# Performance work log

Measured on AMD Instinct MI355X. Metric: run time of the kernel, lower is better.

Reference implementation:

```python
import jax, jax.numpy as jnp
import numpy as np

D, H, BS, K_TOP = 2560, 32, 32, 16
HD = D // H  # 80
B, S = 2, 1024
SCALE = HD ** -0.5


def setup_inputs() -> dict:
    key = jax.random.key(0)
    ks = jax.random.split(key, 10)
    sc = 0.02

    def lin(k, i, o):
        return (jax.random.normal(k, (i, o), jnp.float32) * sc,
                jnp.zeros((o,), jnp.float32))

    Wq, bq = lin(ks[0], D, D)
    Wk, bk = lin(ks[1], D, D)
    Wv, bv = lin(ks[2], D, D)
    Wo, bo = lin(ks[3], D, D)
    comp_W1, comp_b1 = lin(ks[4], BS * HD, 4 * HD)
    comp_W2, comp_b2 = lin(ks[5], 4 * HD, HD)
    comp_pos = jax.random.normal(ks[6], (BS, HD), jnp.float32) * sc
    gate_W1, gate_b1 = lin(ks[7], D, D // 2)
    gate_W2, gate_b2 = lin(ks[8], D // 2, 3)
    hidden_states = jax.random.normal(ks[9], (B, S, D), jnp.float32)
    return dict(hidden_states=hidden_states, Wq=Wq, bq=bq, Wk=Wk, bk=bk,
                Wv=Wv, bv=bv, Wo=Wo, bo=bo, comp_pos=comp_pos,
                comp_W1=comp_W1, comp_b1=comp_b1, comp_W2=comp_W2,
                comp_b2=comp_b2, gate_W1=gate_W1, gate_b1=gate_b1,
                gate_W2=gate_W2, gate_b2=gate_b2)


def reference(hidden_states, Wq, bq, Wk, bk, Wv, bv, Wo, bo, comp_pos,
              comp_W1, comp_b1, comp_W2, comp_b2, gate_W1, gate_b1,
              gate_W2, gate_b2):
    b, s, dm = hidden_states.shape
    blocks = s // BS

    def heads(y):  # [b,s,D] -> [b,H,s,hd]
        return y.reshape(b, s, H, HD).transpose(0, 2, 1, 3)

    q = heads(hidden_states @ Wq + bq)
    k = heads(hidden_states @ Wk + bk)
    v = heads(hidden_states @ Wv + bv)

    # --- compression branch: per-head block compression MLP (shared K/V) ---
    def compress(t):  # [b,H,s,hd] -> [b,H,blocks,hd]
        tb = t.reshape(b, H, blocks, BS, HD) + comp_pos  # pos emb per block slot
        tb = tb.reshape(b, H, blocks, BS * HD)
        h1 = jax.nn.gelu(tb @ comp_W1 + comp_b1, approximate=False)
        return h1 @ comp_W2 + comp_b2

    kc = compress(k)
    vc = compress(v)
    attn_c = jax.nn.softmax(jnp.einsum('bhsd,bhnd->bhsn', q, kc) * SCALE, axis=-1)
    out_c = jnp.einsum('bhsn,bhnd->bhsd', attn_c, vc)

    # --- dense scores, shared by selection scoring and window branch ---
    scores = jnp.einsum('bhqd,bhkd->bhqk', q, k) * SCALE  # [b,H,s,s]

    # --- selection branch: per-query top-k blocks by block-mean score ---
    block_scores = scores.reshape(b, H, s, blocks, BS).mean(-1)  # [b,H,s,blocks]
    _, top_idx = jax.lax.top_k(block_scores, K_TOP)  # [b,H,s,K]
    sel = (jnp.arange(blocks)[None, None, None, None, :] == top_idx[..., None]).any(-2)
    key_mask = jnp.repeat(sel, BS, axis=-1)  # [b,H,s,s]
    sel_scores = jnp.where(key_mask, scores, -jnp.inf)
    out_s = jnp.einsum('bhqk,bhkd->bhqd', jax.nn.softmax(sel_scores, axis=-1), v)

    # --- window branch: source's window mask is all-ones -> full attention ---
    out_w = jnp.einsum('bhqk,bhkd->bhqd', jax.nn.softmax(scores, axis=-1), v)

    # --- learned gates ---
    gh = jax.nn.gelu(hidden_states @ gate_W1 + gate_b1, approximate=False)
    gates = jax.nn.sigmoid(gh @ gate_W2 + gate_b2)  # [b,s,3]
    g = gates.transpose(2, 0, 1)[:, :, None, :, None]  # [3,b,1,s,1]
    combined = g[0] * out_c + g[1] * out_s + g[2] * out_w  # [b,H,s,hd]
    combined = combined.transpose(0, 2, 1, 3).reshape(b, s, dm)
    return combined @ Wo + bo
```

## Files before the change

### kernel.cpp

```cpp
#include <hip/hip_runtime.h>
#include <hip/hip_bf16.h>
#include <math.h>

typedef unsigned short u16;
typedef short v8s __attribute__((ext_vector_type(8)));
typedef float v4f __attribute__((ext_vector_type(4)));

#define SCALE_F 0.11180339887498949f
#define SCALE_L2 0.16129821534f

__device__ __forceinline__ float bf2f(u16 x) {
    unsigned int u = ((unsigned int)x) << 16;
    return __builtin_bit_cast(float, u);
}
__device__ __forceinline__ u16 f2bf(float f) {
    unsigned int u = __builtin_bit_cast(unsigned int, f);
    unsigned int r = (u + 0x7FFFu + ((u >> 16) & 1u)) >> 16;
    return (u16)r;
}
__device__ __forceinline__ float scrub(float v) {
    return (fabsf(v) < 1e30f) ? v : 0.f;
}
__device__ __forceinline__ v8s zero8() {
    union { v8s v; short s[8]; } t;
#pragma unroll
    for (int i = 0; i < 8; i++) t.s[i] = 0;
    return t.v;
}
__device__ __forceinline__ void glds16(const void* g, void* s) {
    __builtin_amdgcn_global_load_lds(
        (const __attribute__((address_space(1))) unsigned int*)g,
        (__attribute__((address_space(3))) unsigned int*)s, 16, 0, 0);
}

__global__ void convX_kernel(const float* __restrict__ X, u16* __restrict__ Xb, int n)
{
    int i = (blockIdx.x * 256 + threadIdx.x) * 4;
    if (i >= n) return;
    float4 v = *(const float4*)(X + i);
    u16 o[4] = { f2bf(v.x), f2bf(v.y), f2bf(v.z), f2bf(v.w) };
    *(uint2*)(Xb + i) = *(uint2*)o;
}

__global__ __launch_bounds__(256) void convT_kernel(
    const float* __restrict__ W, u16* __restrict__ WT, int K, int N)
{
    __shared__ float t[32][33];
    int n0 = blockIdx.x * 32, k0 = blockIdx.y * 32;
    int tx = threadIdx.x & 31, ty = threadIdx.x >> 5;
    for (int i = ty; i < 32; i += 8) {
        int k = k0 + i, n = n0 + tx;
        t[i][tx] = (k < K && n < N) ? W[(size_t)k * N + n] : 0.f;
    }
    __syncthreads();
    for (int i = ty; i < 32; i += 8) {
        int n = n0 + i, k = k0 + tx;
        if (n < N && k < K) WT[(size_t)n * K + k] = f2bf(t[tx][i]);
    }
}

__global__ void xmean_kernel(const float* __restrict__ X, float* __restrict__ Xm)
{
    int c = blockIdx.x * 256 + threadIdx.x;
    if (c >= 2560) return;
    int g = blockIdx.y;
    const float* base = X + (size_t)g * 32 * 2560 + c;
    float s = 0.f;
#pragma unroll 4
    for (int j = 0; j < 32; j++) s += base[(size_t)j * 2560];
    Xm[(size_t)g * 2560 + c] = s * (1.f / 32.f);
}

__global__ __launch_bounds__(256) void gemmS_kernel(
    const float* __restrict__ A, const float* __restrict__ B,
    const float* __restrict__ bias, int M, int N, int K, float* __restrict__ outf)
{
    __shared__ __align__(16) u16 Ah[64][32], Al[64][32];
    __shared__ __align__(16) u16 Bh[64][32], Bl[64][32];
    const int tid = threadIdx.x;
    const int bm = blockIdx.x * 64, bn = blockIdx.y * 64;
    const int w = tid >> 6, lane = tid & 63;
    const int quad = lane >> 4, l = lane & 15;
    v4f acc[4];
#pragma unroll
    for (int nt = 0; nt < 4; nt++)
#pragma unroll
        for (int r = 0; r < 4; r++) acc[nt][r] = 0.f;
    const int ar = tid >> 2, ak = (tid & 3) * 8;
    const int kr = tid >> 3, nc = (tid & 7) * 8;
    for (int k0 = 0; k0 < K; k0 += 32) {
        float4 a0 = *(const float4*)(A + (size_t)(bm + ar) * K + (k0 + ak));
        float4 a1 = *(const float4*)(A + (size_t)(bm + ar) * K + (k0 + ak) + 4);
        float4 b0 = *(const float4*)(B + (size_t)(k0 + kr) * N + (bn + nc));
        float4 b1 = *(const float4*)(B + (size_t)(k0 + kr) * N + (bn + nc) + 4);
        float av[8] = {a0.x,a0.y,a0.z,a0.w,a1.x,a1.y,a1.z,a1.w};
        float bv[8] = {b0.x,b0.y,b0.z,b0.w,b1.x,b1.y,b1.z,b1.w};
        __syncthreads();
#pragma unroll
        for (int j = 0; j < 8; j++) {
            u16 h = f2bf(av[j]);
            Ah[ar][ak + j] = h; Al[ar][ak + j] = f2bf(av[j] - bf2f(h));
            u16 g = f2bf(bv[j]);
            Bh[nc + j][kr] = g; Bl[nc + j][kr] = f2bf(bv[j] - bf2f(g));
        }
        __syncthreads();
        v8s ah = *(const v8s*)(&Ah[w * 16 + l][quad * 8]);
        v8s al = *(const v8s*)(&Al[w * 16 + l][quad * 8]);
#pragma unroll
        for (int nt = 0; nt < 4; nt++) {
            v8s bh = *(const v8s*)(&Bh[nt * 16 + l][quad * 8]);
            v8s bl = *(const v8s*)(&Bl[nt * 16 + l][quad * 8]);
            acc[nt] = __builtin_amdgcn_mfma_f32_16x16x32_bf16(ah, bh, acc[nt], 0, 0, 0);
            acc[nt] = __builtin_amdgcn_mfma_f32_16x16x32_bf16(ah, bl, acc[nt], 0, 0, 0);
            acc[nt] = __builtin_amdgcn_mfma_f32_16x16x32_bf16(al, bh, acc[nt], 0, 0, 0);
        }
    }
#pragma unroll
    for (int nt = 0; nt < 4; nt++) {
        int col = bn + nt * 16 + l;
        float bvs = bias[col];
#pragma unroll
        for (int r = 0; r < 4; r++) {
            int row = bm + w * 16 + quad * 4 + r;
            outf[(size_t)row * N + col] = scrub(acc[nt][r] + bvs);
        }
    }
}

__global__ __launch_bounds__(256) void m1_kernel(
    const float* __restrict__ Wq, const float* __restrict__ km,
    u16* __restrict__ M1hT, u16* __restrict__ M1lT)
{
    __shared__ float Ws[64][81];
    __shared__ float Ks[32][80];
    int k0 = blockIdx.x * 64, h = blockIdx.y, b = blockIdx.z;
    int tid = threadIdx.x;
    for (int i = tid; i < 64 * 80; i += 256) {
        int kk = i / 80, dd = i - kk * 80;
        Ws[kk][dd] = Wq[(size_t)(k0 + kk) * 2560 + h * 80 + dd];
    }
    for (int i = tid; i < 32 * 80; i += 256) {
        int bl = i / 80, dd = i - bl * 80;
        Ks[bl][dd] = km[(size_t)((b << 5) + bl) * 2560 + h * 80 + dd];
    }
    __syncthreads();
    int kk = tid & 63, bq4 = tid >> 6;
    for (int bt = 0; bt < 8; bt++) {
        int blk = bt * 4 + bq4;
        float s = 0.f;
#pragma unroll 8
        for (int d = 0; d < 80; d++) s += Ws[kk][d] * Ks[blk][d];
        u16 hi = f2bf(s);
        size_t o = (size_t)(b * 1024 + h * 32 + blk) * 2560 + k0 + kk;
        M1hT[o] = hi;
        M1lT[o] = f2bf(s - bf2f(hi));
    }
}

__global__ void bias3_kernel(const float* __restrict__ bq, const float* __restrict__ km,
                             float* __restrict__ bias3)
{
    int i = blockIdx.x * 256 + threadIdx.x;
    if (i >= 2048) return;
    int b = i >> 10, hb = i & 1023, h = hb >> 5, blk = hb & 31;
    float s = 0.f;
    for (int d = 0; d < 80; d++) s += bq[h * 80 + d] * km[(size_t)((b << 5) + blk) * 2560 + h * 80 + d];
    bias3[i] = s;
}

__global__ __launch_bounds__(256) void gemmS2_kernel(
    const float* __restrict__ A, const u16* __restrict__ BhT, const u16* __restrict__ BlT,
    const float* __restrict__ bias, int M, int N, int K, float* __restrict__ outf)
{
    __shared__ __align__(16) u16 Ah[64][32], Al[64][32];
    __shared__ __align__(16) u16 Bh[64][32], Bl[64][32];
    const int tid = threadIdx.x;
    const int bm = blockIdx.x * 64, bn = blockIdx.y * 64;
    const int w = tid >> 6, lane = tid & 63;
    const int quad = lane >> 4, l = lane & 15;
    v4f acc[4];
#pragma unroll
    for (int nt = 0; nt < 4; nt++)
#pragma unroll
        for (int r = 0; r < 4; r++) acc[nt][r] = 0.f;
    const int ar = tid >> 2, ak = (tid & 3) * 8;
    for (int k0 = 0; k0 < K; k0 += 32) {
        float4 a0 = *(const float4*)(A + (size_t)(bm + ar) * K + (k0 + ak));
        float4 a1 = *(const float4*)(A + (size_t)(bm + ar) * K + (k0 + ak) + 4);
        float av[8] = {a0.x,a0.y,a0.z,a0.w,a1.x,a1.y,a1.z,a1.w};
        uint4 bh8 = *(const uint4*)(BhT + (size_t)(bn + ar) * K + (k0 + ak));
        uint4 bl8 = *(const uint4*)(BlT + (size_t)(bn + ar) * K + (k0 + ak));
        __syncthreads();
#pragma unroll
        for (int j = 0; j < 8; j++) {
            u16 h = f2bf(av[j]);
            Ah[ar][ak + j] = h; Al[ar][ak + j] = f2bf(av[j] - bf2f(h));
        }
        *(uint4*)(&Bh[ar][ak]) = bh8;
        *(uint4*)(&Bl[ar][ak]) = bl8;
        __syncthreads();
        v8s ah = *(const v8s*)(&Ah[w * 16 + l][quad * 8]);
        v8s al = *(const v8s*)(&Al[w * 16 + l][quad * 8]);
#pragma unroll
        for (int nt = 0; nt < 4; nt++) {
            v8s bh = *(const v8s*)(&Bh[nt * 16 + l][quad * 8]);
            v8s bl = *(const v8s*)(&Bl[nt * 16 + l][quad * 8]);
            acc[nt] = __builtin_amdgcn_mfma_f32_16x16x32_bf16(ah, bh, acc[nt], 0, 0, 0);
            acc[nt] = __builtin_amdgcn_mfma_f32_16x16x32_bf16(ah, bl, acc[nt], 0, 0, 0);
            acc[nt] = __builtin_amdgcn_mfma_f32_16x16x32_bf16(al, bh, acc[nt], 0, 0, 0);
        }
    }
#pragma unroll
    for (int nt = 0; nt < 4; nt++) {
        int col = bn + nt * 16 + l;
        float bvs = bias[col];
#pragma unroll
        for (int r = 0; r < 4; r++) {
            int row = bm + w * 16 + quad * 4 + r;
            outf[(size_t)row * N + col] = scrub(acc[nt][r] + bvs);
        }
    }
}

__global__ __launch_bounds__(256) void gemmB_kernel(
    const u16* __restrict__ A, const u16* __restrict__ Al2, const u16* __restrict__ BT,
    const float* __restrict__ bias, int M, int N, int K, int act, int ldc,
    u16* __restrict__ outb, float* __restrict__ outf, u16* __restrict__ outT)
{
    __shared__ __align__(16) u16 As[64][32];
    __shared__ __align__(16) u16 As2[64][32];
    __shared__ __align__(16) u16 Bs[64][32];
    const int tid = threadIdx.x;
    const int bm = blockIdx.x * 64, bn = blockIdx.y * 64;
    const int w = tid >> 6, lane = tid & 63;
    const int quad = lane >> 4, l = lane & 15;
    v4f acc[4];
#pragma unroll
    for (int nt = 0; nt < 4; nt++)
#pragma unroll
        for (int r = 0; r < 4; r++) acc[nt][r] = 0.f;
    const int ar = tid >> 2, ak = (tid & 3) * 8;
    const int brow = (bn + ar < N) ? (bn + ar) : (N - 1);
    const u16* Ap = A + (size_t)(bm + ar) * K + ak;
    const u16* Bp = BT + (size_t)brow * K + ak;
    const u16* A2p = Al2 ? (Al2 + (size_t)(bm + ar) * K + ak) : nullptr;
    char* AsW  = ((char*)As)  + w * 1024;
    char* As2W = ((char*)As2) + w * 1024;
    char* BsW  = ((char*)Bs)  + w * 1024;
    for (int k0 = 0; k0 < K; k0 += 32) {
        __syncthreads();
        glds16(Ap + k0, AsW);
        glds16(Bp + k0, BsW);
        if (Al2) glds16(A2p + k0, As2W);
        __syncthreads();
        v8s af = *(const v8s*)(&As[w * 16 + l][quad * 8]);
#pragma unroll
        for (int nt = 0; nt < 4; nt++) {
            v8s bf = *(const v8s*)(&Bs[nt * 16 + l][quad * 8]);
            acc[nt] = __builtin_amdgcn_mfma_f32_16x16x32_bf16(af, bf, acc[nt], 0, 0, 0);
        }
        if (Al2) {
            v8s af2 = *(const v8s*)(&As2[w * 16 + l][quad * 8]);
#pragma unroll
            for (int nt = 0; nt < 4; nt++) {
                v8s bf = *(const v8s*)(&Bs[nt * 16 + l][quad * 8]);
                acc[nt] = __builtin_amdgcn_mfma_f32_16x16x32_bf16(af2, bf, acc[nt], 0, 0, 0);
            }
        }
    }
#pragma unroll
    for (int nt = 0; nt < 4; nt++) {
        int col = bn + nt * 16 + l;
        if (col < N) {
            float bvs = bias[col];
#pragma unroll
            for (int r = 0; r < 4; r++) {
                int row = bm + w * 16 + quad * 4 + r;
                float c = acc[nt][r] + bvs;
                if (act == 1) c = 0.5f * c * (1.0f + erff(c * 0.70710678118654752f));
                c = scrub(c);
                if (outf) outf[(size_t)row * ldc + col] = c;
                if (outb) outb[(size_t)row * ldc + col] = f2bf(c);
                if (outT) {
                    int bb = row >> 10, s = row & 1023;
                    int hh = col / 80, dd = col - hh * 80;
                    outT[((size_t)((bb << 5) + hh) * 96 + dd) * 1024 + s] = f2bf(c);
                }
            }
        }
    }
}

__global__ void gatherF_kernel(const u16* __restrict__ src, const float* __restrict__ pos,
                               u16* __restrict__ F)
{
    int row = blockIdx.y;
    int col = blockIdx.x * 256 + threadIdx.x;
    if (col >= 2560) return;
    int b = row >> 10, h = (row >> 5) & 31, blk = row & 31;
    int j = col / 80, d = col - j * 80;
    float v = bf2f(src[(size_t)(b * 1024 + blk * 32 + j) * 2560 + h * 80 + d]) + pos[col];
    F[(size_t)row * 2560 + col] = f2bf(v);
}
__global__ void gatherFT_kernel(const u16* __restrict__ vt, const float* __restrict__ pos,
                                u16* __restrict__ F)
{
    int row = blockIdx.y;
    int col = blockIdx.x * 256 + threadIdx.x;
    if (col >= 2560) return;
    int b = row >> 10, h = (row >> 5) & 31, blk = row & 31;
    int j = col / 80, d = col - j * 80;
    float v = bf2f(vt[((size_t)((b << 5) + h) * 96 + d) * 1024 + blk * 32 + j]) + pos[col];
    F[(size_t)row * 2560 + col] = f2bf(v);
}

__global__ __launch_bounds__(256) void gates_kernel(
    const u16* __restrict__ gh, const float* __restrict__ W2,
    const float* __restrict__ b2, float* __restrict__ gates)
{
    int w = threadIdx.x >> 6, lane = threadIdx.x & 63;
    int token = blockIdx.x * 4 + w;
    float s0 = 0.f, s1 = 0.f, s2 = 0.f;
    for (int i = lane; i < 1280; i += 64) {
        float g = bf2f(gh[(size_t)token * 1280 + i]);
        s0 += g * W2[i * 3 + 0];
        s1 += g * W2[i * 3 + 1];
        s2 += g * W2[i * 3 + 2];
    }
#pragma unroll
    for (int m = 1; m < 64; m <<= 1) {
        s0 += __shfl_xor(s0, m);
        s1 += __shfl_xor(s1, m);
        s2 += __shfl_xor(s2, m);
    }
    if (lane == 0) {
        gates[token * 3 + 0] = scrub(1.f / (1.f + expf(-(s0 + b2[0]))));
        gates[token * 3 + 1] = scrub(1.f / (1.f + expf(-(s1 + b2[1]))));
        gates[token * 3 + 2] = scrub(1.f / (1.f + expf(-(s2 + b2[2]))));
    }
}

__global__ __launch_bounds__(64) void attn_kernel(
    const u16* __restrict__ qb, const u16* __restrict__ kbf,
    const u16* __restrict__ vt, const u16* __restrict__ kc,
    const u16* __restrict__ vc, const float* __restrict__ BSf,
    const float* __restrict__ gates, u16* __restrict__ comb, u16* __restrict__ combl)
{
    const int lane = threadIdx.x, quad = lane >> 4, l = lane & 15;
    const int qt = blockIdx.x, bh = blockIdx.y, b = bh >> 5, h = bh & 31;
    const float NEG = -1e30f;

    __shared__ float bs[16][33];
    __shared__ unsigned int selmask[16];
    __shared__ __align__(16) u16 Pw[16][40];
    __shared__ float ocn[16][80];

    {
        const float* bsrow = BSf + ((size_t)b * 1024 + qt * 16 + l) * 1024 + h * 32 + quad * 8;
#pragma unroll
        for (int i = 0; i < 8; i++) bs[l][quad * 8 + i] = bsrow[i] * SCALE_F;
    }
    __syncthreads();
    if (lane < 16) {
        unsigned int mask = 0u;
        for (int it = 0; it < 16; it++) {
            float best = NEG; int bi = -1;
            for (int n = 0; n < 32; n++) {
                if (((mask >> n) & 1u) == 0u && bs[lane][n] > best) { best = bs[lane][n]; bi = n; }
            }
            if (bi < 0) { for (int n = 0; n < 32; n++) if (((mask >> n) & 1u) == 0u) { bi = n; break; } }
            mask |= (1u << bi);
        }
        selmask[lane] = mask;
    }
    __syncthreads();
    const unsigned int selm_l = selmask[l];
    unsigned int selm[4];
#pragma unroll
    for (int r = 0; r < 4; r++) selm[r] = selmask[quad * 4 + r];

    v8s qfrag[3];
    {
        const u16* qrow = qb + (size_t)(b * 1024 + qt * 16 + l) * 2560 + h * 80;
#pragma unroll
        for (int c = 0; c < 3; c++) {
            if (c == 2 && quad >= 2) { qfrag[c] = zero8(); }
            else qfrag[c] = *(const v8s*)(qrow + c * 32 + quad * 8);
        }
    }

    {
        v4f oc[5];
#pragma unroll
        for (int t = 0; t < 5; t++)
#pragma unroll
            for (int r = 0; r < 4; r++) oc[t][r] = 0.f;
        float l_c[4];
        v4f s0, s1;
#pragma unroll
        for (int r = 0; r < 4; r++) { s0[r] = 0.f; s1[r] = 0.f; }
#pragma unroll
        for (int c = 0; c < 3; c++) {
            v8s b0, b1;
            if (c == 2 && quad >= 2) { b0 = zero8(); b1 = zero8(); }
            else {
                b0 = *(const v8s*)(kc + (size_t)(bh * 32 + l) * 80 + c * 32 + quad * 8);
                b1 = *(const v8s*)(kc + (size_t)(bh * 32 + 16 + l) * 80 + c * 32 + quad * 8);
            }
            s0 = __builtin_amdgcn_mfma_f32_16x16x32_bf16(qfrag[c], b0, s0, 0, 0, 0);
            s1 = __builtin_amdgcn_mfma_f32_16x16x32_bf16(qfrag[c], b1, s1, 0, 0, 0);
        }
#pragma unroll
        for (int r = 0; r < 4; r++) {
            float x0 = s0[r] * SCALE_L2, x1 = s1[r] * SCALE_L2;
            float mx = fmaxf(x0, x1);
#pragma unroll
            for (int m = 1; m < 16; m <<= 1) mx = fmaxf(mx, __shfl_xor(mx, m));
            float p0 = exp2f(x0 - mx), p1 = exp2f(x1 - mx);
            float sm = p0 + p1;
#pragma unroll
            for (int m = 1; m < 16; m <<= 1) sm += __shfl_xor(sm, m);
            l_c[r] = sm;
            Pw[quad * 4 + r][l]      = f2bf(p0);
            Pw[quad * 4 + r][l + 16] = f2bf(p1);
        }
        __syncthreads();
        v8s pa = *(const v8s*)(&Pw[l][quad * 8]);
#pragma unroll
        for (int t = 0; t < 5; t++) {
            union { v8s v; short s[8]; } vf;
#pragma unroll
            for (int j = 0; j < 8; j++)
                vf.s[j] = (short)vc[(size_t)(bh * 32 + quad * 8 + j) * 80 + t * 16 + l];
            oc[t] = __builtin_amdgcn_mfma_f32_16x16x32_bf16(pa, vf.v, oc[t], 0, 0, 0);
        }
#pragma unroll
        for (int r = 0; r < 4; r++) {
            int token = b * 1024 + qt * 16 + quad * 4 + r;
            float g0 = gates[token * 3 + 0];
            float fc = g0 / fmaxf(l_c[r], 1e-30f);
#pragma unroll
            for (int t = 0; t < 5; t++) ocn[quad * 4 + r][t * 16 + l] = oc[t][r] * fc;
        }
        __syncthreads();
    }

    v4f aw[5], as_[5];
    float m_w[4], l_w[4], l_s[4];
#pragma unroll
    for (int r = 0; r < 4; r++) { m_w[r] = NEG; l_w[r] = 0.f; l_s[r] = 0.f; }
#pragma unroll
    for (int t = 0; t < 5; t++)
#pragma unroll
        for (int r = 0; r < 4; r++) { aw[t][r] = 0.f; as_[t][r] = 0.f; }

    const u16* vtp = vt + (size_t)bh * 96 * 1024;

    for (int kb = 0; kb < 32; kb++) {
        v4f s0, s1;
#pragma unroll
        for (int r = 0; r < 4; r++) { s0[r] = 0.f; s1[r] = 0.f; }
#pragma unroll
        for (int c = 0; c < 3; c++) {
            v8s k0f, k1f;
            if (c == 2 && quad >= 2) { k0f = zero8(); k1f = zero8(); }
            else {
                size_t base = (size_t)(b * 1024 + kb * 32) * 2560 + h * 80 + c * 32 + quad * 8;
                k0f = *(const v8s*)(kbf + base + (size_t)l * 2560);
                k1f = *(const v8s*)(kbf + base + (size_t)(16 + l) * 2560);
            }
            s0 = __builtin_amdgcn_mfma_f32_16x16x32_bf16(qfrag[c], k0f, s0, 0, 0, 0);
            s1 = __builtin_amdgcn_mfma_f32_16x16x32_bf16(qfrag[c], k1f, s1, 0, 0, 0);
        }
        float x0a[4], x1a[4], pmax[4];
        float needmax = NEG;
#pragma unroll
        for (int r = 0; r < 4; r++) {
            x0a[r] = s0[r] * SCALE_L2; x1a[r] = s1[r] * SCALE_L2;
            float mb = fmaxf(x0a[r], x1a[r]);
#pragma unroll
            for (int m = 1; m < 16; m <<= 1) mb = fmaxf(mb, __shfl_xor(mb, m));
            pmax[r] = mb;
            needmax = fmaxf(needmax, mb - m_w[r]);
        }
        if (__all(needmax <= 8.0f)) {
#pragma unroll
            for (int r = 0; r < 4; r++) {
                float p0 = exp2f(x0a[r] - m_w[r]), p1 = exp2f(x1a[r] - m_w[r]);
                Pw[quad * 4 + r][l]      = f2bf(p0);
                Pw[quad * 4 + r][l + 16] = f2bf(p1);
                float st = p0 + p1;
#pragma unroll
                for (int m = 1; m < 16; m <<= 1) st += __shfl_xor(st, m);
                l_w[r] += st;
                if ((selm[r] >> kb) & 1u) l_s[r] += st;
            }
        } else {
            float alw[4];
#pragma unroll
            for (int r = 0; r < 4; r++) {
                float mn = fmaxf(m_w[r], pmax[r]);
                alw[r] = exp2f(m_w[r] - mn);
                m_w[r] = mn;
                float p0 = exp2f(x0a[r] - mn), p1 = exp2f(x1a[r] - mn);
                Pw[quad * 4 + r][l]      = f2bf(p0);
                Pw[quad * 4 + r][l + 16] = f2bf(p1);
                float st = p0 + p1;
#pragma unroll
                for (int m = 1; m < 16; m <<= 1) st += __shfl_xor(st, m);
                l_w[r] = l_w[r] * alw[r] + st;
                l_s[r] = l_s[r] * alw[r] + (((selm[r] >> kb) & 1u) ? st : 0.f);
            }
#pragma unroll
            for (int t = 0; t < 5; t++)
#pragma unroll
                for (int r = 0; r < 4; r++) { aw[t][r] *= alw[r]; as_[t][r] *= alw[r]; }
        }
        __syncthreads();
        v8s pwa = *(const v8s*)(&Pw[l][quad * 8]);
        v8s psa = ((selm_l >> kb) & 1u) ? pwa : zero8();
#pragma unroll
        for (int t = 0; t < 5; t++) {
            v8s vfr = *(const v8s*)(vtp + ((size_t)(t * 16 + l)) * 1024 + kb * 32 + quad * 8);
            aw[t]  = __builtin_amdgcn_mfma_f32_16x16x32_bf16(pwa, vfr, aw[t], 0, 0, 0);
            as_[t] = __builtin_amdgcn_mfma_f32_16x16x32_bf16(psa, vfr, as_[t], 0, 0, 0);
        }
        __syncthreads();
    }

#pragma unroll
    for (int r = 0; r < 4; r++) {
        int token = b * 1024 + qt * 16 + quad * 4 + r;
        float g1 = gates[token * 3 + 1], g2 = gates[token * 3 + 2];
        float fw = g2 / fmaxf(l_w[r], 1e-30f);
        float fs = g1 / fmaxf(l_s[r], 1e-30f);
#pragma unroll
        for (int t = 0; t < 5; t++) {
            float val = ocn[quad * 4 + r][t * 16 + l] + fs * as_[t][r] + fw * aw[t][r];
            val = scrub(val);
            u16 hi = f2bf(val);
            size_t o = (size_t)token * 2560 + h * 80 + t * 16 + l;
            comb[o] = hi;
            combl[o] = f2bf(val - bf2f(hi));
        }
    }
}

extern "C" void kernel_launch(void* const* d_in, const int* in_sizes, int n_in,
                              void* d_out, int out_size, void* d_ws, size_t ws_size,
                              hipStream_t stream)
{
    (void)in_sizes; (void)n_in; (void)out_size; (void)ws_size;

    const float* X   = (const float*)d_in[0];
    const float* Wq  = (const float*)d_in[1];
    const float* bq  = (const float*)d_in[2];
    const float* Wk  = (const float*)d_in[3];
    const float* bk  = (const float*)d_in[4];
    const float* Wv  = (const float*)d_in[5];
    const float* bv  = (const float*)d_in[6];
    const float* Wo  = (const float*)d_in[7];
    const float* bo  = (const float*)d_in[8];
    const float* pos = (const float*)d_in[9];
    const float* cW1 = (const float*)d_in[10];
    const float* cb1 = (const float*)d_in[11];
    const float* cW2 = (const float*)d_in[12];
    const float* cb2 = (const float*)d_in[13];
    const float* gW1 = (const float*)d_in[14];
    const float* gb1 = (const float*)d_in[15];
    const float* gW2 = (const float*)d_in[16];
    const float* gb2 = (const float*)d_in[17];

    char* ws = (char*)d_ws;
    size_t off = 0;
    auto alloc = [&](size_t bytes) -> void* {
        void* p = ws + off;
        off += (bytes + 255) & ~(size_t)255;
        return p;
    };
    u16*   Xb     = (u16*)  alloc(2048ull * 2560 * 2);
    u16*   WqT    = (u16*)  alloc(2560ull * 2560 * 2);
    u16*   WkT    = (u16*)  alloc(2560ull * 2560 * 2);
    u16*   WvT    = (u16*)  alloc(2560ull * 2560 * 2);
    u16*   WoT    = (u16*)  alloc(2560ull * 2560 * 2);
    u16*   gW1T   = (u16*)  alloc(1280ull * 2560 * 2);
    u16*   cW1T   = (u16*)  alloc(320ull * 2560 * 2);
    u16*   cW2T   = (u16*)  alloc(96ull * 320 * 2);
    float* Xm     = (float*)alloc(64ull * 2560 * 4);
    float* kmeanS = (float*)alloc(64ull * 2560 * 4);
    u16*   M1hT   = (u16*)  alloc(2048ull * 2560 * 2);
    u16*   M1lT   = (u16*)  alloc(2048ull * 2560 * 2);
    float* bias3  = (float*)alloc(2048ull * 4);
    u16*   qbuf   = (u16*)  alloc(2048ull * 2560 * 2);
    u16*   kbf    = (u16*)  alloc(2048ull * 2560 * 2);
    u16*   vtb    = (u16*)  alloc(64ull * 96 * 1024 * 2);
    u16*   combl  = (u16*)  alloc(2048ull * 2560 * 2);
    char*  R1     = (char*) alloc(12ull * 1024 * 1024);
    u16*   gh     = (u16*)R1;
    u16*   Fb     = (u16*)R1;
    u16*   H1     = (u16*)(R1 + 10ull * 1024 * 1024);
    u16*   combb  = (u16*)R1;
    u16*   KC     = (u16*)  alloc(2048ull * 80 * 2);
    u16*   VC     = (u16*)  alloc(2048ull * 80 * 2);
    float* gatesf = (float*)alloc(2048ull * 3 * 4);
    float* BSf    = (float*)d_out;

    dim3 blk(256);
    convX_kernel<<<2048 * 2560 / 4 / 256, blk, 0, stream>>>(X, Xb, 2048 * 2560);
    convT_kernel<<<dim3(80, 80), blk, 0, stream>>>(Wq, WqT, 2560, 2560);
    convT_kernel<<<dim3(80, 80), blk, 0, stream>>>(Wk, WkT, 2560, 2560);
    convT_kernel<<<dim3(80, 80), blk, 0, stream>>>(Wv, WvT, 2560, 2560);
    convT_kernel<<<dim3(80, 80), blk, 0, stream>>>(Wo, WoT, 2560, 2560);
    convT_kernel<<<dim3(40, 80), blk, 0, stream>>>(gW1, gW1T, 2560, 1280);
    convT_kernel<<<dim3(10, 80), blk, 0, stream>>>(cW1, cW1T, 2560, 320);
    convT_kernel<<<dim3(3, 10), blk, 0, stream>>>(cW2, cW2T, 320, 80);
    xmean_kernel<<<dim3(10, 64), blk, 0, stream>>>(X, Xm);
    gemmS_kernel<<<dim3(1, 40), blk, 0, stream>>>(Xm, Wk, bk, 64, 2560, 2560, kmeanS);
    m1_kernel<<<dim3(40, 32, 2), blk, 0, stream>>>(Wq, kmeanS, M1hT, M1lT);
    bias3_kernel<<<8, blk, 0, stream>>>(bq, kmeanS, bias3);
    for (int b = 0; b < 2; b++) {
        gemmS2_kernel<<<dim3(16, 16), blk, 0, stream>>>(
            X + (size_t)b * 1024 * 2560, M1hT + (size_t)b * 1024 * 2560,
            M1lT + (size_t)b * 1024 * 2560, bias3 + b * 1024,
            1024, 1024, 2560, BSf + (size_t)b * 1024 * 1024);
    }
    gemmB_kernel<<<dim3(32, 40), blk, 0, stream>>>(Xb, nullptr, WqT, bq, 2048, 2560, 2560, 0, 2560, qbuf, nullptr, nullptr);
    gemmB_kernel<<<dim3(32, 40), blk, 0, stream>>>(Xb, nullptr, WkT, bk, 2048, 2560, 2560, 0, 2560, kbf, nullptr, nullptr);
    gemmB_kernel<<<dim3(32, 40), blk, 0, stream>>>(Xb, nullptr, WvT, bv, 2048, 2560, 2560, 0, 2560, nullptr, nullptr, vtb);
    gemmB_kernel<<<dim3(32, 20), blk, 0, stream>>>(Xb, nullptr, gW1T, gb1, 2048, 1280, 2560, 1, 1280, gh, nullptr, nullptr);
    gates_kernel<<<512, blk, 0, stream>>>(gh, gW2, gb2, gatesf);
    gatherF_kernel<<<dim3(10, 2048), blk, 0, stream>>>(kbf, pos, Fb);
    gemmB_kernel<<<dim3(32, 5), blk, 0, stream>>>(Fb, nullptr, cW1T, cb1, 2048, 320, 2560, 1, 320, H1, nullptr, nullptr);
    gemmB_kernel<<<dim3(32, 2), blk, 0, stream>>>(H1, nullptr, cW2T, cb2, 2048, 80, 320, 0, 80, KC, nullptr, nullptr);
    gatherFT_kernel<<<dim3(10, 2048), blk, 0, stream>>>(vtb, pos, Fb);
    gemmB_kernel<<<dim3(32, 5), blk, 0, stream>>>(Fb, nullptr, cW1T, cb1, 2048, 320, 2560, 1, 320, H1, nullptr, nullptr);
    gemmB_kernel<<<dim3(32, 2), blk, 0, stream>>>(H1, nullptr, cW2T, cb2, 2048, 80, 320, 0, 80, VC, nullptr, nullptr);
    attn_kernel<<<dim3(64, 64), 64, 0, stream>>>(qbuf, kbf, vtb, KC, VC, BSf, gatesf, combb, combl);
    gemmB_kernel<<<dim3(32, 40), blk, 0, stream>>>(combb, combl, WoT, bo, 2048, 2560, 2560, 0, 2560, nullptr, (float*)d_out, nullptr);
}
```

Measured before the change: 1.185 ms.

## Add 128x128-tile MFMA GEMM for projections and tune attention priority/occupancy

Adds a new GEMM kernel with 128x128 output tiles, where each of four waves computes a 64x64 sub-tile, and uses it for the Q/K/V, gate and output projections in place of the smaller-tile kernel. Larger tiles increase data reuse per LDS load and cut global traffic. The cost is higher register pressure and fewer blocks per GPU (320 or 160 tiles), which can underfill the CUs. The attention kernel also gets a minimum-occupancy launch bound and s_setprio around its MFMA sections, to help overlap compute across waves.

```diff
diff --git a/kernel.cpp b/kernel.cpp
--- a/kernel.cpp
+++ b/kernel.cpp
@@ -291,6 +291,96 @@
     }
 }
 
+__global__ __launch_bounds__(256) void gemmB128_kernel(
+    const u16* __restrict__ A, const u16* __restrict__ Al2, const u16* __restrict__ BT,
+    const float* __restrict__ bias, int M, int N, int K, int act, int ldc,
+    u16* __restrict__ outb, float* __restrict__ outf, u16* __restrict__ outT)
+{
+    __shared__ __align__(16) u16 As[128][32];
+    __shared__ __align__(16) u16 As2[128][32];
+    __shared__ __align__(16) u16 Bs[128][32];
+    const int tid = threadIdx.x;
+    const int bm = blockIdx.x * 128, bn = blockIdx.y * 128;
+    const int w = tid >> 6, lane = tid & 63;
+    const int quad = lane >> 4, l = lane & 15;
+    const int wr = w >> 1, wc = w & 1;
+    v4f acc[4][4];
+#pragma unroll
+    for (int mt = 0; mt < 4; mt++)
+#pragma unroll
+        for (int nt = 0; nt < 4; nt++)
+#pragma unroll
+            for (int r = 0; r < 4; r++) acc[mt][nt][r] = 0.f;
+    const int r0 = w * 32 + (lane >> 2);
+    const int r1 = r0 + 16;
+    const int kc = (lane & 3) * 8;
+    const u16* Ap0 = A + (size_t)(bm + r0) * K + kc;
+    const u16* Ap1 = A + (size_t)(bm + r1) * K + kc;
+    const u16* Bp0 = BT + (size_t)(bn + r0) * K + kc;
+    const u16* Bp1 = BT + (size_t)(bn + r1) * K + kc;
+    const u16* A2p0 = Al2 ? (Al2 + (size_t)(bm + r0) * K + kc) : nullptr;
+    const u16* A2p1 = Al2 ? (Al2 + (size_t)(bm + r1) * K + kc) : nullptr;
+    char* AsW0  = ((char*)As)  + (w * 2 + 0) * 1024;
+    char* AsW1  = ((char*)As)  + (w * 2 + 1) * 1024;
+    char* BsW0  = ((char*)Bs)  + (w * 2 + 0) * 1024;
+    char* BsW1  = ((char*)Bs)  + (w * 2 + 1) * 1024;
+    char* As2W0 = ((char*)As2) + (w * 2 + 0) * 1024;
+    char* As2W1 = ((char*)As2) + (w * 2 + 1) * 1024;
+    for (int k0 = 0; k0 < K; k0 += 32) {
+        __syncthreads();
+        glds16(Ap0 + k0, AsW0);
+        glds16(Ap1 + k0, AsW1);
+        glds16(Bp0 + k0, BsW0);
+        glds16(Bp1 + k0, BsW1);
+        if (Al2) { glds16(A2p0 + k0, As2W0); glds16(A2p1 + k0, As2W1); }
+        __syncthreads();
+        v8s af[4], bf[4];
+#pragma unroll
+        for (int mt = 0; mt < 4; mt++)
+            af[mt] = *(const v8s*)(&As[wr * 64 + mt * 16 + l][quad * 8]);
+#pragma unroll
+        for (int nt = 0; nt < 4; nt++)
+            bf[nt] = *(const v8s*)(&Bs[wc * 64 + nt * 16 + l][quad * 8]);
+#pragma unroll
+        for (int mt = 0; mt < 4; mt++)
+#pragma unroll
+            for (int nt = 0; nt < 4; nt++)
+                acc[mt][nt] = __builtin_amdgcn_mfma_f32_16x16x32_bf16(af[mt], bf[nt], acc[mt][nt], 0, 0, 0);
+        if (Al2) {
+#pragma unroll
+            for (int mt = 0; mt < 4; mt++) {
+                v8s af2 = *(const v8s*)(&As2[wr * 64 + mt * 16 + l][quad * 8]);
+#pragma unroll
+                for (int nt = 0; nt < 4; nt++)
+                    acc[mt][nt] = __builtin_amdgcn_mfma_f32_16x16x32_bf16(af2, bf[nt], acc[mt][nt], 0, 0, 0);
+            }
+        }
+    }
+#pragma unroll
+    for (int mt = 0; mt < 4; mt++)
+#pragma unroll
+        for (int nt = 0; nt < 4; nt++) {
+            int col = bn + wc * 64 + nt * 16 + l;
+            if (col < N) {
+                float bvs = bias[col];
+#pragma unroll
+                for (int r = 0; r < 4; r++) {
+                    int row = bm + wr * 64 + mt * 16 + quad * 4 + r;
+                    float c = acc[mt][nt][r] + bvs;
+                    if (act == 1) c = 0.5f * c * (1.0f + erff(c * 0.70710678118654752f));
+                    c = scrub(c);
+                    if (outf) outf[(size_t)row * ldc + col] = c;
+                    if (outb) outb[(size_t)row * ldc + col] = f2bf(c);
+                    if (outT) {
+                        int bb = row >> 10, s = row & 1023;
+                        int hh = col / 80, dd = col - hh * 80;
+                        outT[((size_t)((bb << 5) + hh) * 96 + dd) * 1024 + s] = f2bf(c);
+                    }
+                }
+            }
+        }
+}
+
 __global__ void gatherF_kernel(const u16* __restrict__ src, const float* __restrict__ pos,
                                u16* __restrict__ F)
 {
@@ -340,7 +430,7 @@
     }
 }
 
-__global__ __launch_bounds__(64) void attn_kernel(
+__global__ __launch_bounds__(64, 3) void attn_kernel(
     const u16* __restrict__ qb, const u16* __restrict__ kbf,
     const u16* __restrict__ vt, const u16* __restrict__ kc,
     const u16* __restrict__ vc, const float* __restrict__ BSf,
@@ -460,6 +550,7 @@
         v4f s0, s1;
 #pragma unroll
         for (int r = 0; r < 4; r++) { s0[r] = 0.f; s1[r] = 0.f; }
+        __builtin_amdgcn_s_setprio(1);
 #pragma unroll
         for (int c = 0; c < 3; c++) {
             v8s k0f, k1f;
@@ -472,6 +563,7 @@
             s0 = __builtin_amdgcn_mfma_f32_16x16x32_bf16(qfrag[c], k0f, s0, 0, 0, 0);
             s1 = __builtin_amdgcn_mfma_f32_16x16x32_bf16(qfrag[c], k1f, s1, 0, 0, 0);
         }
+        __builtin_amdgcn_s_setprio(0);
         float x0a[4], x1a[4], pmax[4];
         float needmax = NEG;
 #pragma unroll
@@ -519,12 +611,14 @@
         __syncthreads();
         v8s pwa = *(const v8s*)(&Pw[l][quad * 8]);
         v8s psa = ((selm_l >> kb) & 1u) ? pwa : zero8();
+        __builtin_amdgcn_s_setprio(1);
 #pragma unroll
         for (int t = 0; t < 5; t++) {
             v8s vfr = *(const v8s*)(vtp + ((size_t)(t * 16 + l)) * 1024 + kb * 32 + quad * 8);
             aw[t]  = __builtin_amdgcn_mfma_f32_16x16x32_bf16(pwa, vfr, aw[t], 0, 0, 0);
             as_[t] = __builtin_amdgcn_mfma_f32_16x16x32_bf16(psa, vfr, as_[t], 0, 0, 0);
         }
+        __builtin_amdgcn_s_setprio(0);
         __syncthreads();
     }
 
@@ -624,10 +718,10 @@
             M1lT + (size_t)b * 1024 * 2560, bias3 + b * 1024,
             1024, 1024, 2560, BSf + (size_t)b * 1024 * 1024);
     }
-    gemmB_kernel<<<dim3(32, 40), blk, 0, stream>>>(Xb, nullptr, WqT, bq, 2048, 2560, 2560, 0, 2560, qbuf, nullptr, nullptr);
-    gemmB_kernel<<<dim3(32, 40), blk, 0, stream>>>(Xb, nullptr, WkT, bk, 2048, 2560, 2560, 0, 2560, kbf, nullptr, nullptr);
-    gemmB_kernel<<<dim3(32, 40), blk, 0, stream>>>(Xb, nullptr, WvT, bv, 2048, 2560, 2560, 0, 2560, nullptr, nullptr, vtb);
-    gemmB_kernel<<<dim3(32, 20), blk, 0, stream>>>(Xb, nullptr, gW1T, gb1, 2048, 1280, 2560, 1, 1280, gh, nullptr, nullptr);
+    gemmB128_kernel<<<dim3(16, 20), blk, 0, stream>>>(Xb, nullptr, WqT, bq, 2048, 2560, 2560, 0, 2560, qbuf, nullptr, nullptr);
+    gemmB128_kernel<<<dim3(16, 20), blk, 0, stream>>>(Xb, nullptr, WkT, bk, 2048, 2560, 2560, 0, 2560, kbf, nullptr, nullptr);
+    gemmB128_kernel<<<dim3(16, 20), blk, 0, stream>>>(Xb, nullptr, WvT, bv, 2048, 2560, 2560, 0, 2560, nullptr, nullptr, vtb);
+    gemmB128_kernel<<<dim3(16, 10), blk, 0, stream>>>(Xb, nullptr, gW1T, gb1, 2048, 1280, 2560, 1, 1280, gh, nullptr, nullptr);
     gates_kernel<<<512, blk, 0, stream>>>(gh, gW2, gb2, gatesf);
     gatherF_kernel<<<dim3(10, 2048), blk, 0, stream>>>(kbf, pos, Fb);
     gemmB_kernel<<<dim3(32, 5), blk, 0, stream>>>(Fb, nullptr, cW1T, cb1, 2048, 320, 2560, 1, 320, H1, nullptr, nullptr);
@@ -636,5 +730,5 @@
     gemmB_kernel<<<dim3(32, 5), blk, 0, stream>>>(Fb, nullptr, cW1T, cb1, 2048, 320, 2560, 1, 320, H1, nullptr, nullptr);
     gemmB_kernel<<<dim3(32, 2), blk, 0, stream>>>(H1, nullptr, cW2T, cb2, 2048, 80, 320, 0, 80, VC, nullptr, nullptr);
     attn_kernel<<<dim3(64, 64), 64, 0, stream>>>(qbuf, kbf, vtb, KC, VC, BSf, gatesf, combb, combl);
-    gemmB_kernel<<<dim3(32, 40), blk, 0, stream>>>(combb, combl, WoT, bo, 2048, 2560, 2560, 0, 2560, nullptr, (float*)d_out, nullptr);
-}
+    gemmB128_kernel<<<dim3(16, 20), blk, 0, stream>>>(combb, combl, WoT, bo, 2048, 2560, 2560, 0, 2560, nullptr, (float*)d_out, nullptr);
+}
```

Result: slower. 1.351 ms (+14.1%).

## Pack four query-tile waves per attention block and drop block-wide barriers

Applied to the files above, without the earlier changes.

The attention kernel now runs four independent 64-lane waves per 256-thread block, each handling its own 16-query tile with private shared-memory slices. Because all exchange is wave-local, every __syncthreads is removed and the scratch buffers for block scores and the compressed output share one region. s_setprio is raised around the MFMA sections so waves on a SIMD alternate math and softmax. The risks are that removing barriers relies on lockstep execution within a wave for LDS visibility, and that reusing one buffer for both block scores and ocn must stay ordered within the wave.

```diff
diff --git a/kernel.cpp b/kernel.cpp
--- a/kernel.cpp
+++ b/kernel.cpp
@@ -340,40 +340,43 @@
     }
 }
 
-__global__ __launch_bounds__(64) void attn_kernel(
+__global__ __launch_bounds__(256) void attn_kernel(
     const u16* __restrict__ qb, const u16* __restrict__ kbf,
     const u16* __restrict__ vt, const u16* __restrict__ kc,
     const u16* __restrict__ vc, const float* __restrict__ BSf,
     const float* __restrict__ gates, u16* __restrict__ comb, u16* __restrict__ combl)
 {
-    const int lane = threadIdx.x, quad = lane >> 4, l = lane & 15;
-    const int qt = blockIdx.x, bh = blockIdx.y, b = bh >> 5, h = bh & 31;
+    const int tid = threadIdx.x;
+    const int wv = tid >> 6, lane = tid & 63;
+    const int quad = lane >> 4, l = lane & 15;
+    const int qt = blockIdx.x * 4 + wv, bh = blockIdx.y, b = bh >> 5, h = bh & 31;
     const float NEG = -1e30f;
 
-    __shared__ float bs[16][33];
-    __shared__ unsigned int selmask[16];
-    __shared__ __align__(16) u16 Pw[16][40];
-    __shared__ float ocn[16][80];
+    __shared__ float fbuf[4][1344];
+    __shared__ unsigned int selmaskA[4][16];
+    __shared__ __align__(16) u16 PwA[4][16][40];
+    float* bsw = fbuf[wv];
+    float* ocn = fbuf[wv];
+    unsigned int* selmask = selmaskA[wv];
+    u16 (*Pw)[40] = PwA[wv];
 
     {
         const float* bsrow = BSf + ((size_t)b * 1024 + qt * 16 + l) * 1024 + h * 32 + quad * 8;
 #pragma unroll
-        for (int i = 0; i < 8; i++) bs[l][quad * 8 + i] = bsrow[i] * SCALE_F;
-    }
-    __syncthreads();
+        for (int i = 0; i < 8; i++) bsw[l * 33 + quad * 8 + i] = bsrow[i] * SCALE_F;
+    }
     if (lane < 16) {
         unsigned int mask = 0u;
         for (int it = 0; it < 16; it++) {
             float best = NEG; int bi = -1;
             for (int n = 0; n < 32; n++) {
-                if (((mask >> n) & 1u) == 0u && bs[lane][n] > best) { best = bs[lane][n]; bi = n; }
+                if (((mask >> n) & 1u) == 0u && bsw[lane * 33 + n] > best) { best = bsw[lane * 33 + n]; bi = n; }
             }
             if (bi < 0) { for (int n = 0; n < 32; n++) if (((mask >> n) & 1u) == 0u) { bi = n; break; } }
             mask |= (1u << bi);
         }
         selmask[lane] = mask;
     }
-    __syncthreads();
     const unsigned int selm_l = selmask[l];
     unsigned int selm[4];
 #pragma unroll
@@ -424,7 +427,6 @@
             Pw[quad * 4 + r][l]      = f2bf(p0);
             Pw[quad * 4 + r][l + 16] = f2bf(p1);
         }
-        __syncthreads();
         v8s pa = *(const v8s*)(&Pw[l][quad * 8]);
 #pragma unroll
         for (int t = 0; t < 5; t++) {
@@ -440,9 +442,8 @@
             float g0 = gates[token * 3 + 0];
             float fc = g0 / fmaxf(l_c[r], 1e-30f);
 #pragma unroll
-            for (int t = 0; t < 5; t++) ocn[quad * 4 + r][t * 16 + l] = oc[t][r] * fc;
-        }
-        __syncthreads();
+            for (int t = 0; t < 5; t++) ocn[(quad * 4 + r) * 80 + t * 16 + l] = oc[t][r] * fc;
+        }
     }
 
     v4f aw[5], as_[5];
@@ -460,6 +461,7 @@
         v4f s0, s1;
 #pragma unroll
         for (int r = 0; r < 4; r++) { s0[r] = 0.f; s1[r] = 0.f; }
+        __builtin_amdgcn_s_setprio(1);
 #pragma unroll
         for (int c = 0; c < 3; c++) {
             v8s k0f, k1f;
@@ -472,6 +474,7 @@
             s0 = __builtin_amdgcn_mfma_f32_16x16x32_bf16(qfrag[c], k0f, s0, 0, 0, 0);
             s1 = __builtin_amdgcn_mfma_f32_16x16x32_bf16(qfrag[c], k1f, s1, 0, 0, 0);
         }
+        __builtin_amdgcn_s_setprio(0);
         float x0a[4], x1a[4], pmax[4];
         float needmax = NEG;
 #pragma unroll
@@ -516,16 +519,16 @@
 #pragma unroll
                 for (int r = 0; r < 4; r++) { aw[t][r] *= alw[r]; as_[t][r] *= alw[r]; }
         }
-        __syncthreads();
         v8s pwa = *(const v8s*)(&Pw[l][quad * 8]);
         v8s psa = ((selm_l >> kb) & 1u) ? pwa : zero8();
+        __builtin_amdgcn_s_setprio(1);
 #pragma unroll
         for (int t = 0; t < 5; t++) {
             v8s vfr = *(const v8s*)(vtp + ((size_t)(t * 16 + l)) * 1024 + kb * 32 + quad * 8);
             aw[t]  = __builtin_amdgcn_mfma_f32_16x16x32_bf16(pwa, vfr, aw[t], 0, 0, 0);
             as_[t] = __builtin_amdgcn_mfma_f32_16x16x32_bf16(psa, vfr, as_[t], 0, 0, 0);
         }
-        __syncthreads();
+        __builtin_amdgcn_s_setprio(0);
     }
 
 #pragma unroll
@@ -536,7 +539,7 @@
         float fs = g1 / fmaxf(l_s[r], 1e-30f);
 #pragma unroll
         for (int t = 0; t < 5; t++) {
-            float val = ocn[quad * 4 + r][t * 16 + l] + fs * as_[t][r] + fw * aw[t][r];
+            float val = ocn[(quad * 4 + r) * 80 + t * 16 + l] + fs * as_[t][r] + fw * aw[t][r];
             val = scrub(val);
             u16 hi = f2bf(val);
             size_t o = (size_t)token * 2560 + h * 80 + t * 16 + l;
@@ -635,6 +638,6 @@
     gatherFT_kernel<<<dim3(10, 2048), blk, 0, stream>>>(vtb, pos, Fb);
     gemmB_kernel<<<dim3(32, 5), blk, 0, stream>>>(Fb, nullptr, cW1T, cb1, 2048, 320, 2560, 1, 320, H1, nullptr, nullptr);
     gemmB_kernel<<<dim3(32, 2), blk, 0, stream>>>(H1, nullptr, cW2T, cb2, 2048, 80, 320, 0, 80, VC, nullptr, nullptr);
-    attn_kernel<<<dim3(64, 64), 64, 0, stream>>>(qbuf, kbf, vtb, KC, VC, BSf, gatesf, combb, combl);
+    attn_kernel<<<dim3(16, 64), blk, 0, stream>>>(qbuf, kbf, vtb, KC, VC, BSf, gatesf, combb, combl);
     gemmB_kernel<<<dim3(32, 40), blk, 0, stream>>>(combb, combl, WoT, bo, 2048, 2560, 2560, 0, 2560, nullptr, (float*)d_out, nullptr);
 }
```

Result: slower. 1.212 ms (+2.3%).

## Double-buffer LDS tiles in GEMM kernels and batch gemmS2 launches via grid z

Applied to the files above, without the earlier changes.

Both GEMM kernels now keep two LDS tile buffers, prefetching the next K-slice (via direct global-to-LDS loads and register prefetch of the fp32 A operand) while the current slice feeds the MFMAs. This drops one barrier per iteration and hides global load latency. The two per-batch gemmS2 launches are merged into one launch using blockIdx.z. LDS use doubles, which may lower occupancy, and the single trailing barrier must correctly guard buffer reuse.

```diff
diff --git a/kernel.cpp b/kernel.cpp
--- a/kernel.cpp
+++ b/kernel.cpp
@@ -172,8 +172,87 @@
     const float* __restrict__ A, const u16* __restrict__ BhT, const u16* __restrict__ BlT,
     const float* __restrict__ bias, int M, int N, int K, float* __restrict__ outf)
 {
-    __shared__ __align__(16) u16 Ah[64][32], Al[64][32];
-    __shared__ __align__(16) u16 Bh[64][32], Bl[64][32];
+    __shared__ __align__(16) u16 Ah[2][64][32], Al[2][64][32];
+    __shared__ __align__(16) u16 Bh[2][64][32], Bl[2][64][32];
+    const int tid = threadIdx.x;
+    const int z = blockIdx.z;
+    const float* Az = A + (size_t)z * 1024 * 2560;
+    const u16* Bhz = BhT + (size_t)z * 1024 * 2560;
+    const u16* Blz = BlT + (size_t)z * 1024 * 2560;
+    const float* biasz = bias + (size_t)z * 1024;
+    float* outz = outf + (size_t)z * 1024 * 1024;
+    const int bm = blockIdx.x * 64, bn = blockIdx.y * 64;
+    const int w = tid >> 6, lane = tid & 63;
+    const int quad = lane >> 4, l = lane & 15;
+    v4f acc[4];
+#pragma unroll
+    for (int nt = 0; nt < 4; nt++)
+#pragma unroll
+        for (int r = 0; r < 4; r++) acc[nt][r] = 0.f;
+    const int ar = tid >> 2, ak = (tid & 3) * 8;
+    const float* ApF = Az + (size_t)(bm + ar) * K + ak;
+    const u16* BpH = Bhz + (size_t)(bn + ar) * K + ak;
+    const u16* BpL = Blz + (size_t)(bn + ar) * K + ak;
+    char* BhB = (char*)Bh;
+    char* BlB = (char*)Bl;
+    const int NT = K >> 5;
+    glds16(BpH, BhB + w * 1024);
+    glds16(BpL, BlB + w * 1024);
+    float4 a0 = *(const float4*)(ApF);
+    float4 a1 = *(const float4*)(ApF + 4);
+    __syncthreads();
+    for (int t = 0; t < NT; t++) {
+        const int cur = t & 1;
+        const int nxt = cur ^ 1;
+        if (t + 1 < NT) {
+            int k0n = (t + 1) << 5;
+            glds16(BpH + k0n, BhB + nxt * 4096 + w * 1024);
+            glds16(BpL + k0n, BlB + nxt * 4096 + w * 1024);
+        }
+        float av[8] = {a0.x, a0.y, a0.z, a0.w, a1.x, a1.y, a1.z, a1.w};
+        if (t + 1 < NT) {
+            int k0n = (t + 1) << 5;
+            a0 = *(const float4*)(ApF + k0n);
+            a1 = *(const float4*)(ApF + k0n + 4);
+        }
+#pragma unroll
+        for (int j = 0; j < 8; j++) {
+            u16 h = f2bf(av[j]);
+            Ah[cur][ar][ak + j] = h;
+            Al[cur][ar][ak + j] = f2bf(av[j] - bf2f(h));
+        }
+        v8s ah = *(const v8s*)(&Ah[cur][w * 16 + l][quad * 8]);
+        v8s al2 = *(const v8s*)(&Al[cur][w * 16 + l][quad * 8]);
+#pragma unroll
+        for (int nt = 0; nt < 4; nt++) {
+            v8s bh = *(const v8s*)(&Bh[cur][nt * 16 + l][quad * 8]);
+            v8s bl = *(const v8s*)(&Bl[cur][nt * 16 + l][quad * 8]);
+            acc[nt] = __builtin_amdgcn_mfma_f32_16x16x32_bf16(ah, bh, acc[nt], 0, 0, 0);
+            acc[nt] = __builtin_amdgcn_mfma_f32_16x16x32_bf16(ah, bl, acc[nt], 0, 0, 0);
+            acc[nt] = __builtin_amdgcn_mfma_f32_16x16x32_bf16(al2, bh, acc[nt], 0, 0, 0);
+        }
+        __syncthreads();
+    }
+#pragma unroll
+    for (int nt = 0; nt < 4; nt++) {
+        int col = bn + nt * 16 + l;
+        float bvs = biasz[col];
+#pragma unroll
+        for (int r = 0; r < 4; r++) {
+            int row = bm + w * 16 + quad * 4 + r;
+            outz[(size_t)row * N + col] = scrub(acc[nt][r] + bvs);
+        }
+    }
+}
+
+__global__ __launch_bounds__(256) void gemmB_kernel(
+    const u16* __restrict__ A, const u16* __restrict__ Al2, const u16* __restrict__ BT,
+    const float* __restrict__ bias, int M, int N, int K, int act, int ldc,
+    u16* __restrict__ outb, float* __restrict__ outf, u16* __restrict__ outT)
+{
+    __shared__ __align__(16) u16 As[2][64][32];
+    __shared__ __align__(16) u16 As2[2][64][32];
+    __shared__ __align__(16) u16 Bs[2][64][32];
     const int tid = threadIdx.x;
     const int bm = blockIdx.x * 64, bn = blockIdx.y * 64;
     const int w = tid >> 6, lane = tid & 63;
@@ -183,90 +262,44 @@
     for (int nt = 0; nt < 4; nt++)
 #pragma unroll
         for (int r = 0; r < 4; r++) acc[nt][r] = 0.f;
-    const int ar = tid >> 2, ak = (tid & 3) * 8;
-    for (int k0 = 0; k0 < K; k0 += 32) {
-        float4 a0 = *(const float4*)(A + (size_t)(bm + ar) * K + (k0 + ak));
-        float4 a1 = *(const float4*)(A + (size_t)(bm + ar) * K + (k0 + ak) + 4);
-        float av[8] = {a0.x,a0.y,a0.z,a0.w,a1.x,a1.y,a1.z,a1.w};
-        uint4 bh8 = *(const uint4*)(BhT + (size_t)(bn + ar) * K + (k0 + ak));
-        uint4 bl8 = *(const uint4*)(BlT + (size_t)(bn + ar) * K + (k0 + ak));
-        __syncthreads();
-#pragma unroll
-        for (int j = 0; j < 8; j++) {
-            u16 h = f2bf(av[j]);
-            Ah[ar][ak + j] = h; Al[ar][ak + j] = f2bf(av[j] - bf2f(h));
-        }
-        *(uint4*)(&Bh[ar][ak]) = bh8;
-        *(uint4*)(&Bl[ar][ak]) = bl8;
-        __syncthreads();
-        v8s ah = *(const v8s*)(&Ah[w * 16 + l][quad * 8]);
-        v8s al = *(const v8s*)(&Al[w * 16 + l][quad * 8]);
+    const int srow = w * 16 + (lane >> 2);
+    const int kcol = (lane & 3) * 8;
+    const int brow = (bn + srow < N) ? (bn + srow) : (N - 1);
+    const u16* Ap = A + (size_t)(bm + srow) * K + kcol;
+    const u16* Bp = BT + (size_t)brow * K + kcol;
+    const u16* A2p = Al2 ? (Al2 + (size_t)(bm + srow) * K + kcol) : nullptr;
+    char* AsB = (char*)As;
+    char* As2B = (char*)As2;
+    char* BsB = (char*)Bs;
+    const int NT = K >> 5;
+    glds16(Ap, AsB + w * 1024);
+    glds16(Bp, BsB + w * 1024);
+    if (Al2) glds16(A2p, As2B + w * 1024);
+    __syncthreads();
+    for (int t = 0; t < NT; t++) {
+        const int cur = t & 1;
+        const int nxt = cur ^ 1;
+        if (t + 1 < NT) {
+            int k0n = (t + 1) << 5;
+            glds16(Ap + k0n, AsB + nxt * 4096 + w * 1024);
+            glds16(Bp + k0n, BsB + nxt * 4096 + w * 1024);
+            if (Al2) glds16(A2p + k0n, As2B + nxt * 4096 + w * 1024);
+        }
+        v8s af = *(const v8s*)(&As[cur][w * 16 + l][quad * 8]);
 #pragma unroll
         for (int nt = 0; nt < 4; nt++) {
-            v8s bh = *(const v8s*)(&Bh[nt * 16 + l][quad * 8]);
-            v8s bl = *(const v8s*)(&Bl[nt * 16 + l][quad * 8]);
-            acc[nt] = __builtin_amdgcn_mfma_f32_16x16x32_bf16(ah, bh, acc[nt], 0, 0, 0);
-            acc[nt] = __builtin_amdgcn_mfma_f32_16x16x32_bf16(ah, bl, acc[nt], 0, 0, 0);
-            acc[nt] = __builtin_amdgcn_mfma_f32_16x16x32_bf16(al, bh, acc[nt], 0, 0, 0);
-        }
-    }
-#pragma unroll
-    for (int nt = 0; nt < 4; nt++) {
-        int col = bn + nt * 16 + l;
-        float bvs = bias[col];
-#pragma unroll
-        for (int r = 0; r < 4; r++) {
-            int row = bm + w * 16 + quad * 4 + r;
-            outf[(size_t)row * N + col] = scrub(acc[nt][r] + bvs);
-        }
-    }
-}
-
-__global__ __launch_bounds__(256) void gemmB_kernel(
-    const u16* __restrict__ A, const u16* __restrict__ Al2, const u16* __restrict__ BT,
-    const float* __restrict__ bias, int M, int N, int K, int act, int ldc,
-    u16* __restrict__ outb, float* __restrict__ outf, u16* __restrict__ outT)
-{
-    __shared__ __align__(16) u16 As[64][32];
-    __shared__ __align__(16) u16 As2[64][32];
-    __shared__ __align__(16) u16 Bs[64][32];
-    const int tid = threadIdx.x;
-    const int bm = blockIdx.x * 64, bn = blockIdx.y * 64;
-    const int w = tid >> 6, lane = tid & 63;
-    const int quad = lane >> 4, l = lane & 15;
-    v4f acc[4];
-#pragma unroll
-    for (int nt = 0; nt < 4; nt++)
-#pragma unroll
-        for (int r = 0; r < 4; r++) acc[nt][r] = 0.f;
-    const int ar = tid >> 2, ak = (tid & 3) * 8;
-    const int brow = (bn + ar < N) ? (bn + ar) : (N - 1);
-    const u16* Ap = A + (size_t)(bm + ar) * K + ak;
-    const u16* Bp = BT + (size_t)brow * K + ak;
-    const u16* A2p = Al2 ? (Al2 + (size_t)(bm + ar) * K + ak) : nullptr;
-    char* AsW  = ((char*)As)  + w * 1024;
-    char* As2W = ((char*)As2) + w * 1024;
-    char* BsW  = ((char*)Bs)  + w * 1024;
-    for (int k0 = 0; k0 < K; k0 += 32) {
-        __syncthreads();
-        glds16(Ap + k0, AsW);
-        glds16(Bp + k0, BsW);
-        if (Al2) glds16(A2p + k0, As2W);
-        __syncthreads();
-        v8s af = *(const v8s*)(&As[w * 16 + l][quad * 8]);
-#pragma unroll
-        for (int nt = 0; nt < 4; nt++) {
-            v8s bf = *(const v8s*)(&Bs[nt * 16 + l][quad * 8]);
+            v8s bf = *(const v8s*)(&Bs[cur][nt * 16 + l][quad * 8]);
             acc[nt] = __builtin_amdgcn_mfma_f32_16x16x32_bf16(af, bf, acc[nt], 0, 0, 0);
         }
         if (Al2) {
-            v8s af2 = *(const v8s*)(&As2[w * 16 + l][quad * 8]);
+            v8s af2 = *(const v8s*)(&As2[cur][w * 16 + l][quad * 8]);
 #pragma unroll
             for (int nt = 0; nt < 4; nt++) {
-                v8s bf = *(const v8s*)(&Bs[nt * 16 + l][quad * 8]);
+                v8s bf = *(const v8s*)(&Bs[cur][nt * 16 + l][quad * 8]);
                 acc[nt] = __builtin_amdgcn_mfma_f32_16x16x32_bf16(af2, bf, acc[nt], 0, 0, 0);
             }
         }
+        __syncthreads();
     }
 #pragma unroll
     for (int nt = 0; nt < 4; nt++) {
@@ -618,12 +651,7 @@
     gemmS_kernel<<<dim3(1, 40), blk, 0, stream>>>(Xm, Wk, bk, 64, 2560, 2560, kmeanS);
     m1_kernel<<<dim3(40, 32, 2), blk, 0, stream>>>(Wq, kmeanS, M1hT, M1lT);
     bias3_kernel<<<8, blk, 0, stream>>>(bq, kmeanS, bias3);
-    for (int b = 0; b < 2; b++) {
-        gemmS2_kernel<<<dim3(16, 16), blk, 0, stream>>>(
-            X + (size_t)b * 1024 * 2560, M1hT + (size_t)b * 1024 * 2560,
-            M1lT + (size_t)b * 1024 * 2560, bias3 + b * 1024,
-            1024, 1024, 2560, BSf + (size_t)b * 1024 * 1024);
-    }
+    gemmS2_kernel<<<dim3(16, 16, 2), blk, 0, stream>>>(X, M1hT, M1lT, bias3, 1024, 1024, 2560, BSf);
     gemmB_kernel<<<dim3(32, 40), blk, 0, stream>>>(Xb, nullptr, WqT, bq, 2048, 2560, 2560, 0, 2560, qbuf, nullptr, nullptr);
     gemmB_kernel<<<dim3(32, 40), blk, 0, stream>>>(Xb, nullptr, WkT, bk, 2048, 2560, 2560, 0, 2560, kbf, nullptr, nullptr);
     gemmB_kernel<<<dim3(32, 40), blk, 0, stream>>>(Xb, nullptr, WvT, bv, 2048, 2560, 2560, 0, 2560, nullptr, nullptr, vtb);
```

Result: faster. 1.137 ms (-4.0%).
